# Kernel tuning notes

Hardware: AMD Instinct MI355X
Metric: run time of the kernel (lower is better)

The kernel has to match this reference:

```python
import jax, jax.numpy as jnp
import numpy as np

# Config (mirrors init_kwargs)
N_PARTS = 4
N_DATASETS = 4
N_VOLUMES = 12
N_TRANSFORMS = 1
TEMP = 0.1
EPS = 1e-6
BS = N_PARTS * N_DATASETS * N_VOLUMES          # 192
N = BS * (N_TRANSFORMS + 1)                    # 384 total rows
PD = N_PARTS * N_DATASETS                      # 16
C, H, W = 32, 48, 48


def setup_inputs() -> dict:
    key = jax.random.key(0)
    k1, k2 = jax.random.split(key)
    reg_pred = jax.random.normal(k1, (N, C, H, W), dtype=jnp.float32)
    mean_representations = jax.random.normal(k2, (N_DATASETS, C, H, W), dtype=jnp.float32)
    return {"reg_pred": reg_pred, "mean_representations": mean_representations}


def reference(reg_pred, mean_representations):
    X = reg_pred.reshape(N, -1)                                  # [N, D]
    ds_id = (jnp.arange(N) // N_PARTS) % N_DATASETS              # dataset id per row
    Mn = mean_representations.reshape(N_DATASETS, -1)[ds_id]     # [N, D] per-row mean
    Z = X - Mn                                                   # demeaned
    # cosine similarity with per-vector norm clamped at eps (torch CosineSimilarity)
    nrm = jnp.maximum(jnp.linalg.norm(Z, axis=1), EPS)
    Zn = Z / nrm[:, None]
    S = (Zn @ Zn.T) / TEMP                                       # [N, N] scaled cos sims
    E = jnp.exp(S)
    # negative (denominator) set for anchor a: all j with j % PD != a % PD
    rem = jnp.arange(N) % PD
    neg_mask = rem[:, None] != rem[None, :]
    Dsum = jnp.sum(E * neg_mask, axis=1)                         # [N]

    p = jnp.arange(BS)
    i1 = p
    i2 = BS + p
    i3 = (p + PD) % N
    i4 = (BS + p + PD) % N

    def pair_loss(a, b):
        # Faithful to original: BOTH terms use the (a,b) numerator similarity
        num = S[a, b]
        en = jnp.exp(num)
        return -(num - jnp.log(en + Dsum[a])) - (num - jnp.log(en + Dsum[b]))

    total = (pair_loss(i1, i2) + pair_loss(i3, i4)
             + pair_loss(i1, i3) + pair_loss(i2, i4)).sum()
    return total / (N_TRANSFORMS * 3 * BS)
```

## Files before the change

kernel.cpp:

```cpp
#include <hip/hip_runtime.h>
#include <hip/hip_bf16.h>
#include <stdint.h>

#define NR 384
#define DD 73728
#define PDV 16
#define BSV 192
#define KSPLIT 128
#define KCH 576
#define BK 32
#define NIT 18
#define RS 40

typedef __bf16 bf16;
typedef __attribute__((ext_vector_type(4))) __bf16 bf16x4;
typedef __attribute__((ext_vector_type(8))) __bf16 bf16x8;
typedef __attribute__((ext_vector_type(4))) float f32x4;

__global__ __launch_bounds__(256, 3) void k_gram(const float* __restrict__ X,
                                                 const float* __restrict__ M,
                                                 float* __restrict__ Gp) {
    __shared__ float msh[4 * KCH];
    __shared__ bf16 ash[128 * RS];
    __shared__ bf16 bsh[128 * RS];
    const int tid  = threadIdx.x;
    const int lane = tid & 63;
    const int w    = tid >> 6;
    const int quad = lane >> 4;
    const int l15  = lane & 15;
    const int wm   = w & 1, wn = w >> 1;
    const int srow = tid >> 3;
    const int fseg = tid & 7;

    int tile = blockIdx.x % 6;
    int ks   = blockIdx.x / 6;
    int tm = (tile < 3) ? 0 : ((tile < 5) ? 1 : 2);
    int tn = (tile < 3) ? tile : ((tile < 5) ? (tile - 2) : 2);
    const bool diag = (tm == tn);
    const float* Xa = X + (size_t)(tm * 128) * DD;
    const float* Xb = X + (size_t)(tn * 128) * DD;
    const bf16* bbase = diag ? ash : bsh;
    size_t k0 = (size_t)ks * KCH;

    for (int i = tid; i < 4 * 144; i += 256) {
        int ds = i / 144;
        int c  = (i - ds * 144) * 4;
        *(float4*)&msh[ds * KCH + c] = *(const float4*)(M + (size_t)ds * DD + k0 + c);
    }

    f32x4 acc[4][4];
#pragma unroll
    for (int i = 0; i < 4; ++i)
#pragma unroll
        for (int j = 0; j < 4; ++j) acc[i][j] = (f32x4){0.f, 0.f, 0.f, 0.f};

    float4 xa[4], xb[4];
    auto load_regs = [&](int it) {
        size_t gk = k0 + (size_t)it * BK + fseg * 4;
#pragma unroll
        for (int p = 0; p < 4; ++p) {
            int row = p * 32 + srow;
            xa[p] = *(const float4*)(Xa + (size_t)row * DD + gk);
            if (!diag) xb[p] = *(const float4*)(Xb + (size_t)row * DD + gk);
        }
    };
    auto write_tiles = [&](int it) {
        int kc = it * BK + fseg * 4;
#pragma unroll
        for (int p = 0; p < 4; ++p) {
            int row = p * 32 + srow;
            float4 m4 = *(const float4*)&msh[((row >> 2) & 3) * KCH + kc];
            bf16x4 za;
            za[0] = (bf16)(xa[p].x - m4.x); za[1] = (bf16)(xa[p].y - m4.y);
            za[2] = (bf16)(xa[p].z - m4.z); za[3] = (bf16)(xa[p].w - m4.w);
            *(bf16x4*)&ash[row * RS + fseg * 4] = za;
            if (!diag) {
                bf16x4 zb;
                zb[0] = (bf16)(xb[p].x - m4.x); zb[1] = (bf16)(xb[p].y - m4.y);
                zb[2] = (bf16)(xb[p].z - m4.z); zb[3] = (bf16)(xb[p].w - m4.w);
                *(bf16x4*)&bsh[row * RS + fseg * 4] = zb;
            }
        }
    };

    load_regs(0);
    __syncthreads();
    write_tiles(0);

    for (int it = 0; it < NIT; ++it) {
        __syncthreads();
        if (it + 1 < NIT) load_regs(it + 1);
        bf16x8 af[4], bfv[4];
#pragma unroll
        for (int i = 0; i < 4; ++i) {
            int r = wm * 64 + i * 16 + l15;
            af[i] = *(const bf16x8*)&ash[r * RS + quad * 8];
        }
#pragma unroll
        for (int j = 0; j < 4; ++j) {
            int r = wn * 64 + j * 16 + l15;
            bfv[j] = *(const bf16x8*)&bbase[r * RS + quad * 8];
        }
#pragma unroll
        for (int i = 0; i < 4; ++i)
#pragma unroll
            for (int j = 0; j < 4; ++j)
                acc[i][j] = __builtin_amdgcn_mfma_f32_16x16x32_bf16(
                    af[i], bfv[j], acc[i][j], 0, 0, 0);
        __syncthreads();
        if (it + 1 < NIT) write_tiles(it + 1);
    }

    float* gp = Gp + ((size_t)(ks * 6 + tile) << 14);
#pragma unroll
    for (int i = 0; i < 4; ++i) {
        int lr0 = wm * 64 + i * 16 + quad * 4;
#pragma unroll
        for (int j = 0; j < 4; ++j) {
            int lc = wn * 64 + j * 16 + l15;
#pragma unroll
            for (int r = 0; r < 4; ++r)
                gp[(lr0 + r) * 128 + lc] = acc[i][j][r];
        }
    }
}

__global__ __launch_bounds__(256) void k_red(const float* __restrict__ Gp,
                                             float* __restrict__ G,
                                             float* __restrict__ invn,
                                             float* __restrict__ out) {
    int t    = blockIdx.x * 256 + threadIdx.x;
    if (t == 0) out[0] = 0.0f;
    int tile = t >> 14;
    int idx  = t & 16383;
    int lr   = idx >> 7, lc = idx & 127;
    const float* p = Gp + ((size_t)tile << 14) + idx;
    float s = 0.0f;
#pragma unroll 8
    for (int ks = 0; ks < KSPLIT; ++ks) s += p[(size_t)ks * 98304];
    int tm = (tile < 3) ? 0 : ((tile < 5) ? 1 : 2);
    int tn = (tile < 3) ? tile : ((tile < 5) ? (tile - 2) : 2);
    int a = tm * 128 + lr, b = tn * 128 + lc;
    G[(size_t)a * NR + b] = s;
    G[(size_t)b * NR + a] = s;
    if (a == b) invn[a] = 1.0f / fmaxf(sqrtf(s), 1e-6f);
}

__global__ __launch_bounds__(256) void k_dsum(const float* __restrict__ G,
                                              const float* __restrict__ invn,
                                              float* __restrict__ out) {
    const int lane = threadIdx.x & 63;
    const int a    = blockIdx.x * 4 + (threadIdx.x >> 6);
    float ia  = invn[a];
    int arem  = a & 15;
    float acc = 0.0f;
    for (int b = lane; b < NR; b += 64) {
        float s = G[(size_t)a * NR + b] * ia * invn[b] * 10.0f;
        if ((b & 15) != arem) acc += expf(s);
    }
#pragma unroll
    for (int o = 32; o > 0; o >>= 1) acc += __shfl_down(acc, o);
    if (lane == 0) {
        float Dsa = acc;
        int pr[4];
        if (a < 16)       { pr[0] = 192 + a; pr[1] = a + 16;  pr[2] = a + 192; pr[3] = a + 368; }
        else if (a < 192) { pr[0] = 192 + a; pr[1] = a + 16;  pr[2] = a + 192; pr[3] = a - 16; }
        else if (a < 368) { pr[0] = a - 192; pr[1] = a + 16;  pr[2] = a - 192; pr[3] = a - 16; }
        else              { pr[0] = a - 192; pr[1] = a - 368; pr[2] = a - 192; pr[3] = a - 16; }
        float t = 0.0f;
#pragma unroll
        for (int s = 0; s < 4; ++s) {
            int b = pr[s];
            float num = G[(size_t)a * NR + b] * ia * invn[b] * 10.0f;
            t += -num + logf(expf(num) + Dsa);
        }
        atomicAdd(out, t * (1.0f / 576.0f));
    }
}

extern "C" void kernel_launch(void* const* d_in, const int* in_sizes, int n_in,
                              void* d_out, int out_size, void* d_ws, size_t ws_size,
                              hipStream_t stream) {
    const float* X = (const float*)d_in[0];
    const float* M = (const float*)d_in[1];
    float* out = (float*)d_out;

    char* ws = (char*)d_ws;
    float* Gp   = (float*)ws;
    float* G    = Gp + (size_t)KSPLIT * 6 * 16384;
    float* invn = G + (size_t)NR * NR;

    k_gram<<<dim3(6 * KSPLIT), dim3(256), 0, stream>>>(X, M, Gp);
    k_red<<<dim3(384), dim3(256), 0, stream>>>(Gp, G, invn, out);
    k_dsum<<<dim3(NR / 4), dim3(256), 0, stream>>>(G, invn, out);
}
```

Before: 197.8 us.

## Double-buffer global loads in registers and remap blocks to XCDs by k-split

The gram kernel now keeps two register buffers of global X loads, so each load is issued two iterations ahead of its use instead of one, which gives more memory latency hiding. The block-to-(tile, k-split) mapping is also changed so that the six tiles sharing a k-chunk land on the same XCD, aiming for better L2 reuse of the X rows and mean chunk. The extra register buffers increase VGPR pressure and may lower occupancy under the 3-blocks-per-CU launch bound.

```diff
diff --git a/kernel.cpp b/kernel.cpp
--- a/kernel.cpp
+++ b/kernel.cpp
@@ -32,8 +32,10 @@
     const int srow = tid >> 3;
     const int fseg = tid & 7;
 
-    int tile = blockIdx.x % 6;
-    int ks   = blockIdx.x / 6;
+    int xcd  = blockIdx.x & 7;
+    int g    = blockIdx.x >> 3;
+    int tile = g % 6;
+    int ks   = xcd + 8 * (g / 6);
     int tm = (tile < 3) ? 0 : ((tile < 5) ? 1 : 2);
     int tn = (tile < 3) ? tile : ((tile < 5) ? (tile - 2) : 2);
     const bool diag = (tm == tn);
@@ -54,8 +56,8 @@
 #pragma unroll
         for (int j = 0; j < 4; ++j) acc[i][j] = (f32x4){0.f, 0.f, 0.f, 0.f};
 
-    float4 xa[4], xb[4];
-    auto load_regs = [&](int it) {
+    float4 xa0[4], xb0[4], xa1[4], xb1[4];
+    auto load_regs = [&](int it, float4 (&xa)[4], float4 (&xb)[4]) {
         size_t gk = k0 + (size_t)it * BK + fseg * 4;
 #pragma unroll
         for (int p = 0; p < 4; ++p) {
@@ -64,7 +66,7 @@
             if (!diag) xb[p] = *(const float4*)(Xb + (size_t)row * DD + gk);
         }
     };
-    auto write_tiles = [&](int it) {
+    auto write_tiles = [&](int it, float4 (&xa)[4], float4 (&xb)[4]) {
         int kc = it * BK + fseg * 4;
 #pragma unroll
         for (int p = 0; p < 4; ++p) {
@@ -82,14 +84,7 @@
             }
         }
     };
-
-    load_regs(0);
-    __syncthreads();
-    write_tiles(0);
-
-    for (int it = 0; it < NIT; ++it) {
-        __syncthreads();
-        if (it + 1 < NIT) load_regs(it + 1);
+    auto compute = [&]() {
         bf16x8 af[4], bfv[4];
 #pragma unroll
         for (int i = 0; i < 4; ++i) {
@@ -107,8 +102,24 @@
             for (int j = 0; j < 4; ++j)
                 acc[i][j] = __builtin_amdgcn_mfma_f32_16x16x32_bf16(
                     af[i], bfv[j], acc[i][j], 0, 0, 0);
-        __syncthreads();
-        if (it + 1 < NIT) write_tiles(it + 1);
+    };
+
+    load_regs(0, xa0, xb0);
+    load_regs(1, xa1, xb1);
+    __syncthreads();
+    write_tiles(0, xa0, xb0);
+
+    for (int it = 0; it < NIT; it += 2) {
+        __syncthreads();
+        if (it + 2 < NIT) load_regs(it + 2, xa0, xb0);
+        compute();
+        __syncthreads();
+        write_tiles(it + 1, xa1, xb1);
+        __syncthreads();
+        if (it + 3 < NIT) load_regs(it + 3, xa1, xb1);
+        compute();
+        __syncthreads();
+        if (it + 2 < NIT) write_tiles(it + 2, xa0, xb0);
     }
 
     float* gp = Gp + ((size_t)(ks * 6 + tile) << 14);
```

After: 202.7 us. 1.02x slower.

## Double-buffer LDS tiles in gram kernel and remap blocks across XCDs

Applied to the files above, without the earlier changes.

Double-buffers the shared-memory A/B tiles so each iteration needs one barrier instead of two. The next tile is written and the global loads two steps ahead are issued before the MFMA compute on the current buffer, so memory latency overlaps math. Block indices are remapped so that consecutive k-splits land on the same XCD with all six output tiles, aiming for better L2 reuse of X rows. The per-row mean vector is now loaded once per iteration instead of once per row. The extra LDS buffers and prefetch registers may reduce occupancy.

```diff
diff --git a/kernel.cpp b/kernel.cpp
--- a/kernel.cpp
+++ b/kernel.cpp
@@ -21,8 +21,8 @@
                                                  const float* __restrict__ M,
                                                  float* __restrict__ Gp) {
     __shared__ float msh[4 * KCH];
-    __shared__ bf16 ash[128 * RS];
-    __shared__ bf16 bsh[128 * RS];
+    __shared__ bf16 ash[2][128 * RS];
+    __shared__ bf16 bsh[2][128 * RS];
     const int tid  = threadIdx.x;
     const int lane = tid & 63;
     const int w    = tid >> 6;
@@ -31,15 +31,17 @@
     const int wm   = w & 1, wn = w >> 1;
     const int srow = tid >> 3;
     const int fseg = tid & 7;
-
-    int tile = blockIdx.x % 6;
-    int ks   = blockIdx.x / 6;
+    const int mds  = (srow >> 2) & 3;
+
+    int xcd  = blockIdx.x & 7;
+    int g    = blockIdx.x >> 3;
+    int tile = g % 6;
+    int ks   = xcd + 8 * (g / 6);
     int tm = (tile < 3) ? 0 : ((tile < 5) ? 1 : 2);
     int tn = (tile < 3) ? tile : ((tile < 5) ? (tile - 2) : 2);
     const bool diag = (tm == tn);
     const float* Xa = X + (size_t)(tm * 128) * DD;
     const float* Xb = X + (size_t)(tn * 128) * DD;
-    const bf16* bbase = diag ? ash : bsh;
     size_t k0 = (size_t)ks * KCH;
 
     for (int i = tid; i < 4 * 144; i += 256) {
@@ -64,42 +66,36 @@
             if (!diag) xb[p] = *(const float4*)(Xb + (size_t)row * DD + gk);
         }
     };
-    auto write_tiles = [&](int it) {
+    auto write_tiles = [&](int it, int buf) {
         int kc = it * BK + fseg * 4;
+        float4 m4 = *(const float4*)&msh[mds * KCH + kc];
 #pragma unroll
         for (int p = 0; p < 4; ++p) {
             int row = p * 32 + srow;
-            float4 m4 = *(const float4*)&msh[((row >> 2) & 3) * KCH + kc];
             bf16x4 za;
             za[0] = (bf16)(xa[p].x - m4.x); za[1] = (bf16)(xa[p].y - m4.y);
             za[2] = (bf16)(xa[p].z - m4.z); za[3] = (bf16)(xa[p].w - m4.w);
-            *(bf16x4*)&ash[row * RS + fseg * 4] = za;
+            *(bf16x4*)&ash[buf][row * RS + fseg * 4] = za;
             if (!diag) {
                 bf16x4 zb;
                 zb[0] = (bf16)(xb[p].x - m4.x); zb[1] = (bf16)(xb[p].y - m4.y);
                 zb[2] = (bf16)(xb[p].z - m4.z); zb[3] = (bf16)(xb[p].w - m4.w);
-                *(bf16x4*)&bsh[row * RS + fseg * 4] = zb;
+                *(bf16x4*)&bsh[buf][row * RS + fseg * 4] = zb;
             }
         }
     };
-
-    load_regs(0);
-    __syncthreads();
-    write_tiles(0);
-
-    for (int it = 0; it < NIT; ++it) {
-        __syncthreads();
-        if (it + 1 < NIT) load_regs(it + 1);
+    auto compute = [&](int buf) {
+        const bf16* bb = diag ? ash[buf] : bsh[buf];
         bf16x8 af[4], bfv[4];
 #pragma unroll
         for (int i = 0; i < 4; ++i) {
             int r = wm * 64 + i * 16 + l15;
-            af[i] = *(const bf16x8*)&ash[r * RS + quad * 8];
+            af[i] = *(const bf16x8*)&ash[buf][r * RS + quad * 8];
         }
 #pragma unroll
         for (int j = 0; j < 4; ++j) {
             int r = wn * 64 + j * 16 + l15;
-            bfv[j] = *(const bf16x8*)&bbase[r * RS + quad * 8];
+            bfv[j] = *(const bf16x8*)&bb[r * RS + quad * 8];
         }
 #pragma unroll
         for (int i = 0; i < 4; ++i)
@@ -107,8 +103,22 @@
             for (int j = 0; j < 4; ++j)
                 acc[i][j] = __builtin_amdgcn_mfma_f32_16x16x32_bf16(
                     af[i], bfv[j], acc[i][j], 0, 0, 0);
+    };
+
+    load_regs(0);
+    __syncthreads();
+    write_tiles(0, 0);
+    load_regs(1);
+    __syncthreads();
+
+    for (int it = 0; it < NIT; ++it) {
+        int buf = it & 1;
+        if (it + 1 < NIT) {
+            write_tiles(it + 1, buf ^ 1);
+            if (it + 2 < NIT) load_regs(it + 2);
+        }
+        compute(buf);
         __syncthreads();
-        if (it + 1 < NIT) write_tiles(it + 1);
     }
 
     float* gp = Gp + ((size_t)(ks * 6 + tile) << 14);
```

New measurement: 195.1 us. No clear change (-1.4%).
